# Performance work log

Hardware: AMD Instinct MI355X
Metric: run time of the kernel (lower is better)

The kernel has to match this reference:

```python
import jax, jax.numpy as jnp
import numpy as np

N = 100000   # nodes
E = 3200000  # edges (avg degree 32)
H = 75       # hidden
ITER = 3     # num_layers


def setup_inputs() -> dict:
    key = jax.random.key(0)
    ks = jax.random.split(key, 16)
    s = 0.1  # weight scale
    x = jax.random.normal(ks[0], (N, H), jnp.float32)
    src = jax.random.randint(ks[1], (E,), 0, N)
    dst = jax.random.randint(ks[2], (E,), 0, N)
    edge_index = jnp.stack([src, dst]).astype(jnp.int32)
    rn = lambda k, shp: jax.random.normal(k, shp, jnp.float32) * s
    return {
        "x": x,
        "edge_index": edge_index,
        "eps": jnp.zeros((1,), jnp.float32),      # GIN train_eps, init 0
        "w1": rn(ks[3], (H, H)), "b1": jnp.zeros((H,), jnp.float32),
        "w2": rn(ks[4], (H, H)), "b2": jnp.zeros((H,), jnp.float32),
        "w_ih": rn(ks[5], (3 * H, H)), "w_hh": rn(ks[6], (3 * H, H)),
        "b_ih": jnp.zeros((3 * H,), jnp.float32), "b_hh": jnp.zeros((3 * H,), jnp.float32),
        "wc1": rn(ks[7], (ITER * H, 2 * H)), "bc1": jnp.zeros((2 * H,), jnp.float32),
        "wc2": rn(ks[8], (2 * H, H)), "bc2": jnp.zeros((H,), jnp.float32),
    }


def reference(x, edge_index, eps, w1, b1, w2, b2, w_ih, w_hh, b_ih, b_hh, wc1, bc1, wc2, bc2):
    src, dst = edge_index[0], edge_index[1]

    def gin(xt):
        # sum aggregation over incoming edges (gather -> scatter-add)
        agg = jax.ops.segment_sum(xt[src], dst, num_segments=N)
        z = (1.0 + eps[0]) * xt + agg
        return jnp.maximum(z @ w1 + b1, 0.0) @ w2 + b2

    def gru_step(inp, h):
        # torch.nn.GRU single step; gate order: r, z, n
        gi = inp @ w_ih.T + b_ih
        gh = h @ w_hh.T + b_hh
        ir, iz, inn = jnp.split(gi, 3, axis=-1)
        hr, hz, hn = jnp.split(gh, 3, axis=-1)
        r = jax.nn.sigmoid(ir + hr)
        zg = jax.nn.sigmoid(iz + hz)
        n = jnp.tanh(inn + r * hn)
        return (1.0 - zg) * n + zg * h

    h = x   # h0 = x.unsqueeze(0)
    xt = x
    node_states = []
    for _ in range(ITER):
        m = jnp.maximum(gin(xt), 0.0)
        h = gru_step(m, h)
        xt = h  # GRU output == hidden state for single layer/step
        node_states.append(xt)

    cat = jnp.concatenate(node_states, axis=1)  # [N, ITER*H]
    readout = jnp.maximum(cat @ wc1 + bc1, 0.0) @ wc2 + bc2
    return (xt, readout)
```

## Files before the change

kernel.cpp:

```cpp
#include <hip/hip_runtime.h>

#define NN 100000
#define EE 3200000
#define N2 100032
#define NBUCK 782
#define CPAD 16
#define CHUNK 12288
#define CAP 5120

typedef _Float16 f16;
typedef _Float16 f16x8 __attribute__((ext_vector_type(8)));
typedef float f32x4 __attribute__((ext_vector_type(4)));
typedef unsigned int u32;

#define MFMA(a, b, c) __builtin_amdgcn_mfma_f32_16x16x32_f16((a), (b), (c), 0, 0, 0)


__global__ __launch_bounds__(256) void initcur_kernel(int* __restrict__ bcur) {
  int i = blockIdx.x * 256 + threadIdx.x;
  if (i < NBUCK) bcur[i * CPAD] = i * CAP;
}

__global__ __launch_bounds__(256) void binB_kernel(const int* __restrict__ src,
                                                   const int* __restrict__ dst,
                                                   int* __restrict__ bcur,
                                                   u32* __restrict__ ebuf) {
  __shared__ int hist[NBUCK];
  __shared__ int base[NBUCK];
  int tid = threadIdx.x;
  int e0 = blockIdx.x * CHUNK;
  int e1 = e0 + CHUNK;
  if (e1 > EE) e1 = EE;
  for (int i = tid; i < NBUCK; i += 256) hist[i] = 0;
  __syncthreads();
  for (int e = e0 + tid * 4; e < e1; e += 1024) {
    int4 d = *(const int4*)(dst + e);
    atomicAdd(&hist[d.x >> 7], 1);
    atomicAdd(&hist[d.y >> 7], 1);
    atomicAdd(&hist[d.z >> 7], 1);
    atomicAdd(&hist[d.w >> 7], 1);
  }
  __syncthreads();
  for (int i = tid; i < NBUCK; i += 256) {
    int c = hist[i];
    if (c) base[i] = atomicAdd(&bcur[i * CPAD], c);
  }
  __syncthreads();
  for (int i = tid; i < NBUCK; i += 256) hist[i] = 0;
  __syncthreads();
  for (int e = e0 + tid * 4; e < e1; e += 1024) {
    int4 d = *(const int4*)(dst + e);
    int4 s = *(const int4*)(src + e);
    int b, loc;
    b = d.x >> 7; loc = atomicAdd(&hist[b], 1);
    ebuf[base[b] + loc] = (u32)s.x | ((u32)(d.x & 127) << 17);
    b = d.y >> 7; loc = atomicAdd(&hist[b], 1);
    ebuf[base[b] + loc] = (u32)s.y | ((u32)(d.y & 127) << 17);
    b = d.z >> 7; loc = atomicAdd(&hist[b], 1);
    ebuf[base[b] + loc] = (u32)s.z | ((u32)(d.z & 127) << 17);
    b = d.w >> 7; loc = atomicAdd(&hist[b], 1);
    ebuf[base[b] + loc] = (u32)s.w | ((u32)(d.w & 127) << 17);
  }
}

__global__ __launch_bounds__(256) void binC_kernel(const u32* __restrict__ ebuf,
                                                   const int* __restrict__ bcur,
                                                   int* __restrict__ st,
                                                   int* __restrict__ ct,
                                                   int* __restrict__ csr) {
  __shared__ int cnt[128], sc[128], cur[128];
  int b = blockIdx.x, tid = threadIdx.x;
  int e0 = b * CAP;
  int e1 = bcur[b * CPAD];
  if (tid < 128) cnt[tid] = 0;
  __syncthreads();
  for (int e = e0 + tid; e < e1; e += 256) atomicAdd(&cnt[ebuf[e] >> 17], 1);
  __syncthreads();
  if (tid < 128) sc[tid] = cnt[tid];
  __syncthreads();
  for (int off = 1; off < 128; off <<= 1) {
    int t = 0;
    if (tid < 128 && tid >= off) t = sc[tid - off];
    __syncthreads();
    if (tid < 128) sc[tid] += t;
    __syncthreads();
  }
  if (tid < 128) {
    int gpos = e0 + sc[tid] - cnt[tid];
    int node = b * 128 + tid;
    if (node < NN) {
      st[node] = gpos;
      ct[node] = cnt[tid];
    }
    cur[tid] = gpos;
  }
  __syncthreads();
  for (int e = e0 + tid; e < e1; e += 256) {
    u32 p = ebuf[e];
    int pos = atomicAdd(&cur[p >> 17], 1);
    csr[pos] = (int)(p & 0x1FFFFu);
  }
}


__device__ __forceinline__ f16 pack_one(const float* __restrict__ W,
                                        const float* __restrict__ bias, int rel, int K, int Nc,
                                        int KG, int trans, int bslot) {
  int e = rel & 7, nn = (rel >> 3) & 15;
  int g = (rel >> 7) % KG, nb = (rel >> 7) / KG;
  int k = g * 8 + e, n = nb * 16 + nn;
  float v = 0.f;
  if (n < Nc) {
    if (k < K) v = trans ? W[n * K + k] : W[k * Nc + n];
    else if (k == bslot) v = bias[n];
  }
  return (f16)v;
}

__global__ __launch_bounds__(256) void prep_kernel(const float* __restrict__ x,
                                                   f16* __restrict__ xp,
                                                   const float* __restrict__ w1,
                                                   const float* __restrict__ b1,
                                                   const float* __restrict__ w2,
                                                   const float* __restrict__ b2,
                                                   const float* __restrict__ wih,
                                                   const float* __restrict__ bih,
                                                   const float* __restrict__ whh,
                                                   const float* __restrict__ bhh,
                                                   const float* __restrict__ wc1,
                                                   const float* __restrict__ bc1,
                                                   const float* __restrict__ wc2,
                                                   const float* __restrict__ bc2,
                                                   f16* __restrict__ wp) {
  int b = blockIdx.x, tid = threadIdx.x;
  if (b < 470) {
    int i = b * 256 + tid;
    if (i >= 120320) return;
    f16 v;
    if (i < 7680) v = pack_one(w1, b1, i, 75, 75, 12, 0, 95);
    else if (i < 15360) v = pack_one(w2, b2, i - 7680, 75, 75, 12, 0, 95);
    else if (i < 38400) {
      int r = i - 15360, g = r / 7680;
      v = pack_one(wih + g * 5625, bih + g * 75, r - g * 7680, 75, 75, 12, 1, 95);
    } else if (i < 61440) {
      int r = i - 38400, g = r / 7680;
      v = pack_one(whh + g * 5625, bhh + g * 75, r - g * 7680, 75, 75, 12, 1, 95);
    } else if (i < 107520) {
      int rel = i - 61440;
      int e = rel & 7, nn = (rel >> 3) & 15;
      int g = (rel >> 7) % 36, nb = (rel >> 7) / 36;
      int q = g * 8 + e, buf = q / 96, kk = q - buf * 96, n = nb * 16 + nn;
      float f = 0.f;
      if (n < 150) {
        if (kk < 75) f = wc1[(buf * 75 + kk) * 150 + n];
        else if (kk == 95 && buf == 0) f = bc1[n];
      }
      v = (f16)f;
    } else v = pack_one(wc2, bc2, i - 107520, 150, 75, 20, 0, 159);
    wp[i] = v;
  } else {
    int i = (b - 470) * 256 + tid;
    int r = i / 96, c = i - r * 96;
    float v = (r < NN && c < 75) ? x[r * 75 + c] : (c == 95 ? 1.f : 0.f);
    xp[i] = (f16)v;
  }
}


__global__ __launch_bounds__(256) void fuse_kernel(const f16* __restrict__ hcur,
                                                   const int* __restrict__ st,
                                                   const int* __restrict__ ct,
                                                   const int* __restrict__ csr,
                                                   const float* __restrict__ eps,
                                                   const f16* __restrict__ w1p,
                                                   const f16* __restrict__ w2p,
                                                   const f16* __restrict__ wihp,
                                                   const f16* __restrict__ whhp,
                                                   f16* __restrict__ hb_out,
                                                   float* __restrict__ outx) {
  __shared__ f16 Ls[4][16 * 104];
  __shared__ f16 Hs[4][16 * 104];
  int tid = threadIdx.x;
  int w = tid >> 6, l = tid & 63, lm = l & 15, lg = l >> 4;
  int row0 = blockIdx.x * 64 + w * 16;
  f16* Ld = Ls[w];
  int g = l / 10, j = l - g * 10;
  float ep = 1.f + eps[0];
#pragma unroll 1
  for (int r = 0; r < 3; ++r) {
    int idx = r * 6 + g;
    if (g < 6 && idx < 16) {
      int n = row0 + idx;
      bool valid = n < NN;
      int e = valid ? st[n] : 0;
      int eend = e + (valid ? ct[n] : 0);
      float acc[8] = {0, 0, 0, 0, 0, 0, 0, 0};
#pragma unroll 4
      for (; e < eend; ++e) {
        int sr = csr[e];
        f16x8 v = *(const f16x8*)(hcur + sr * 96 + j * 8);
#pragma unroll
        for (int k = 0; k < 8; ++k) acc[k] += (float)v[k];
      }
      f16x8 o;
      if (valid) {
        f16x8 self = *(const f16x8*)(hcur + n * 96 + j * 8);
#pragma unroll
        for (int k = 0; k < 8; ++k) o[k] = (f16)(ep * (float)self[k] + acc[k]);
      } else {
#pragma unroll
        for (int k = 0; k < 8; ++k) o[k] = (f16)0.f;
      }
      *(f16x8*)(Ld + idx * 104 + j * 8) = o;
    }
  }
#pragma unroll
  for (int c = 0; c < 4; ++c) {
    int col = 80 + lg * 4 + c;
    Ld[lm * 104 + col] = (f16)(col == 95 ? 1.f : 0.f);
  }
  const f16* hr = hcur + (row0 + lm) * 96;
  f16x8 h0 = *(const f16x8*)(hr + lg * 8);
  f16x8 h1 = *(const f16x8*)(hr + 32 + lg * 8);
  f16x8 h2 = *(const f16x8*)(hr + 64 + lg * 8);
  f16* Hd = Hs[w];
  *(f16x8*)(Hd + lm * 104 + lg * 8) = h0;
  *(f16x8*)(Hd + lm * 104 + 32 + lg * 8) = h1;
  *(f16x8*)(Hd + lm * 104 + 64 + lg * 8) = h2;
  const f16* Lr = Ld + lm * 104;
  f16x8 a0 = *(const f16x8*)(Lr + lg * 8);
  f16x8 a1 = *(const f16x8*)(Lr + 32 + lg * 8);
  f16x8 a2 = *(const f16x8*)(Lr + 64 + lg * 8);
#pragma unroll
  for (int nb = 0; nb < 5; ++nb) {
    const f16* bp = w1p + ((nb * 12 + lg) * 16 + lm) * 8;
    f32x4 acc = (f32x4){0.f, 0.f, 0.f, 0.f};
    acc = MFMA(a0, *(const f16x8*)bp, acc);
    acc = MFMA(a1, *(const f16x8*)(bp + 512), acc);
    acc = MFMA(a2, *(const f16x8*)(bp + 1024), acc);
#pragma unroll
    for (int r = 0; r < 4; ++r)
      Ld[(lg * 4 + r) * 104 + nb * 16 + lm] = (f16)fmaxf(acc[r], 0.f);
  }
  f16x8 c0 = *(const f16x8*)(Lr + lg * 8);
  f16x8 c1 = *(const f16x8*)(Lr + 32 + lg * 8);
  f16x8 c2 = *(const f16x8*)(Lr + 64 + lg * 8);
#pragma unroll
  for (int nb = 0; nb < 5; ++nb) {
    const f16* bp = w2p + ((nb * 12 + lg) * 16 + lm) * 8;
    f32x4 acc = (f32x4){0.f, 0.f, 0.f, 0.f};
    acc = MFMA(c0, *(const f16x8*)bp, acc);
    acc = MFMA(c1, *(const f16x8*)(bp + 512), acc);
    acc = MFMA(c2, *(const f16x8*)(bp + 1024), acc);
#pragma unroll
    for (int r = 0; r < 4; ++r)
      Ld[(lg * 4 + r) * 104 + nb * 16 + lm] = (f16)fmaxf(acc[r], 0.f);
  }
  f16x8 am0 = *(const f16x8*)(Lr + lg * 8);
  f16x8 am1 = *(const f16x8*)(Lr + 32 + lg * 8);
  f16x8 am2 = *(const f16x8*)(Lr + 64 + lg * 8);
#pragma unroll 1
  for (int nb = 0; nb < 5; ++nb) {
    f32x4 rg = (f32x4){0.f, 0.f, 0.f, 0.f};
    f32x4 zg = rg, ni = rg, nh = rg;
#pragma unroll
    for (int s = 0; s < 3; ++s) {
      f16x8 ams = (s == 0) ? am0 : (s == 1) ? am1 : am2;
      f16x8 ahs = (s == 0) ? h0 : (s == 1) ? h1 : h2;
      int fo = ((nb * 12 + s * 4 + lg) * 16 + lm) * 8;
      rg = MFMA(ams, *(const f16x8*)(wihp + fo), rg);
      rg = MFMA(ahs, *(const f16x8*)(whhp + fo), rg);
      zg = MFMA(ams, *(const f16x8*)(wihp + 7680 + fo), zg);
      zg = MFMA(ahs, *(const f16x8*)(whhp + 7680 + fo), zg);
      ni = MFMA(ams, *(const f16x8*)(wihp + 15360 + fo), ni);
      nh = MFMA(ahs, *(const f16x8*)(whhp + 15360 + fo), nh);
    }
#pragma unroll
    for (int r = 0; r < 4; ++r) {
      int n = nb * 16 + lm;
      float hval = (float)Hd[(lg * 4 + r) * 104 + n];
      float rv = 1.f / (1.f + __expf(-rg[r]));
      float zv = 1.f / (1.f + __expf(-zg[r]));
      float u = ni[r] + rv * nh[r];
      float t = __expf(-2.f * fabsf(u));
      float nv = copysignf((1.f - t) / (1.f + t), u);
      float hp = zv * (hval - nv) + nv;
      Ld[(lg * 4 + r) * 104 + n] = (f16)hp;
    }
  }
#pragma unroll
  for (int k = 0; k < 3; ++k) {
    int p = l + 64 * k;
    int r = p / 12, sl = p - r * 12;
    f16x8 v = *(const f16x8*)(Ld + r * 104 + sl * 8);
    *(f16x8*)(hb_out + (row0 + r) * 96 + sl * 8) = v;
  }
  if (outx) {
    for (int k = 0; k < 19; ++k) {
      int p = l + 64 * k;
      int gi = row0 * 75 + p;
      if (p < 1200 && gi < NN * 75) {
        int r = p / 75, c = p - r * 75;
        outx[gi] = (float)Ld[r * 104 + c];
      }
    }
  }
}


__global__ __launch_bounds__(256) void readout_kernel(const f16* __restrict__ hb0,
                                                      const f16* __restrict__ hb1,
                                                      const f16* __restrict__ hb2,
                                                      const f16* __restrict__ wc1p,
                                                      const f16* __restrict__ wc2p,
                                                      float* __restrict__ out) {
  __shared__ f16 Ls[4][16 * 168];
  int tid = threadIdx.x;
  int w = tid >> 6, l = tid & 63, lm = l & 15, lg = l >> 4;
  int row0 = blockIdx.x * 64 + w * 16;
  int row = row0 + lm;
  f16x8 a[9];
#pragma unroll
  for (int s = 0; s < 9; ++s) {
    const f16* hb = (s < 3) ? hb0 : (s < 6) ? hb1 : hb2;
    a[s] = *(const f16x8*)(hb + row * 96 + (4 * (s - (s / 3) * 3) + lg) * 8);
  }
  f16* Ld = Ls[w];
#pragma unroll
  for (int nb = 0; nb < 10; ++nb) {
    f32x4 acc = (f32x4){0.f, 0.f, 0.f, 0.f};
#pragma unroll
    for (int s = 0; s < 9; ++s)
      acc = MFMA(a[s], *(const f16x8*)(wc1p + ((nb * 36 + 4 * s + lg) * 16 + lm) * 8), acc);
#pragma unroll
    for (int r = 0; r < 4; ++r) {
      int n = nb * 16 + lm;
      float v = fmaxf(acc[r], 0.f);
      if (n >= 150) v = (n == 159) ? 1.f : 0.f;
      Ld[(lg * 4 + r) * 168 + n] = (f16)v;
    }
  }
  const f16* Lr = Ls[w] + lm * 168;
  f16x8 a2[5];
#pragma unroll
  for (int s = 0; s < 5; ++s) a2[s] = *(const f16x8*)(Lr + s * 32 + lg * 8);
  f32x4 acc2[5];
#pragma unroll
  for (int nb = 0; nb < 5; ++nb) {
    acc2[nb] = (f32x4){0.f, 0.f, 0.f, 0.f};
#pragma unroll
    for (int s = 0; s < 5; ++s)
      acc2[nb] = MFMA(a2[s], *(const f16x8*)(wc2p + ((nb * 20 + s * 4 + lg) * 16 + lm) * 8),
                      acc2[nb]);
  }
  float* Lf = (float*)Ls[w];
#pragma unroll
  for (int nb = 0; nb < 5; ++nb)
#pragma unroll
    for (int r = 0; r < 4; ++r) {
      int n = nb * 16 + lm;
      if (n < 75) Lf[(lg * 4 + r) * 76 + n] = acc2[nb][r];
    }
  for (int k = 0; k < 19; ++k) {
    int p = l + 64 * k;
    int gi = row0 * 75 + p;
    if (p < 1200 && gi < NN * 75) {
      int r = p / 75, c = p - r * 75;
      out[gi] = Lf[r * 76 + c];
    }
  }
}


extern "C" void kernel_launch(void* const* d_in, const int* in_sizes, int n_in,
                              void* d_out, int out_size, void* d_ws, size_t ws_size,
                              hipStream_t stream) {
  const float* x    = (const float*)d_in[0];
  const int*   ei   = (const int*)d_in[1];
  const float* eps  = (const float*)d_in[2];
  const float* w1   = (const float*)d_in[3];
  const float* b1   = (const float*)d_in[4];
  const float* w2   = (const float*)d_in[5];
  const float* b2   = (const float*)d_in[6];
  const float* w_ih = (const float*)d_in[7];
  const float* w_hh = (const float*)d_in[8];
  const float* b_ih = (const float*)d_in[9];
  const float* b_hh = (const float*)d_in[10];
  const float* wc1  = (const float*)d_in[11];
  const float* bc1  = (const float*)d_in[12];
  const float* wc2  = (const float*)d_in[13];
  const float* bc2  = (const float*)d_in[14];

  const int* srcv = ei;
  const int* dstv = ei + EE;

  float* out_x = (float*)d_out;
  float* out_r = out_x + NN * 75;

  f16* x0   = (f16*)d_ws;
  f16* hb0  = x0 + (size_t)N2 * 96;
  f16* hb1  = hb0 + (size_t)N2 * 96;
  f16* hb2  = hb1 + (size_t)N2 * 96;
  f16* wp   = hb2 + (size_t)N2 * 96;
  f16* w1p  = wp;
  f16* w2p  = wp + 7680;
  f16* wihp = wp + 15360;
  f16* whhp = wp + 38400;
  f16* wc1p = wp + 61440;
  f16* wc2p = wp + 107520;
  u32* ebuf = (u32*)(wp + 120320);
  int* csr  = (int*)(ebuf + (size_t)NBUCK * CAP);
  int* st   = csr + (size_t)NBUCK * CAP;
  int* ctv  = st + NN;
  int* bcur = ctv + NN;

  initcur_kernel<<<4, 256, 0, stream>>>(bcur);
  binB_kernel<<<(EE + CHUNK - 1) / CHUNK, 256, 0, stream>>>(srcv, dstv, bcur, ebuf);
  binC_kernel<<<NBUCK, 256, 0, stream>>>(ebuf, bcur, st, ctv, csr);
  prep_kernel<<<37982, 256, 0, stream>>>(x, x0, w1, b1, w2, b2, w_ih, b_ih,
                                         w_hh, b_hh, wc1, bc1, wc2, bc2, wp);

  int gb = N2 / 64;
  f16* hbs[3] = {hb0, hb1, hb2};
  for (int it = 0; it < 3; ++it) {
    const f16* h = (it == 0) ? x0 : hbs[it - 1];
    fuse_kernel<<<gb, 256, 0, stream>>>(h, st, ctv, csr, eps, w1p, w2p, wihp, whhp,
                                        hbs[it], (it == 2) ? out_x : nullptr);
  }
  readout_kernel<<<gb, 256, 0, stream>>>(hb0, hb1, hb2, wc1p, wc2p, out_r);
}
```

Baseline: 544.5 us.

## Split fused GIN layer into edge-parallel aggregation and MLP/GRU kernels

```diff
diff --git a/kernel.cpp b/kernel.cpp
--- a/kernel.cpp
+++ b/kernel.cpp
@@ -119,6 +119,8 @@
 
 __global__ __launch_bounds__(256) void prep_kernel(const float* __restrict__ x,
                                                    f16* __restrict__ xp,
+                                                   f16* __restrict__ xc,
+                                                   f16* __restrict__ zm,
                                                    const float* __restrict__ w1,
                                                    const float* __restrict__ b1,
                                                    const float* __restrict__ w2,
@@ -158,68 +160,86 @@
       v = (f16)f;
     } else v = pack_one(wc2, bc2, i - 107520, 150, 75, 20, 0, 159);
     wp[i] = v;
-  } else {
+  } else if (b < 6722) {
     int i = (b - 470) * 256 + tid;
+    int r = i >> 4, c = i & 15;
+    zm[r * 96 + 80 + c] = (f16)(c == 15 ? 1.f : 0.f);
+  } else if (b < 44234) {
+    int i = (b - 6722) * 256 + tid;
     int r = i / 96, c = i - r * 96;
     float v = (r < NN && c < 75) ? x[r * 75 + c] : (c == 95 ? 1.f : 0.f);
     xp[i] = (f16)v;
-  }
-}
-
-
-__global__ __launch_bounds__(256) void fuse_kernel(const f16* __restrict__ hcur,
+  } else {
+    int i = (b - 44234) * 256 + tid;
+    int r = i / 80, c = i - r * 80;
+    float v = (r < NN && c < 75) ? x[r * 75 + c] : 0.f;
+    xc[i] = (f16)v;
+  }
+}
+
+
+__global__ __launch_bounds__(256) void aggz_kernel(const f16* __restrict__ xc,
                                                    const int* __restrict__ st,
                                                    const int* __restrict__ ct,
                                                    const int* __restrict__ csr,
                                                    const float* __restrict__ eps,
-                                                   const f16* __restrict__ w1p,
-                                                   const f16* __restrict__ w2p,
-                                                   const f16* __restrict__ wihp,
-                                                   const f16* __restrict__ whhp,
-                                                   f16* __restrict__ hb_out,
-                                                   float* __restrict__ outx) {
+                                                   f16* __restrict__ zm) {
+  int tid = threadIdx.x;
+  int l = tid & 63;
+  int n = blockIdx.x * 4 + (tid >> 6);
+  if (n >= NN) return;
+  int s = l / 10, j = l - s * 10;
+  int e0 = st[n], e1 = e0 + ct[n];
+  float acc[8] = {0, 0, 0, 0, 0, 0, 0, 0};
+  if (l < 60) {
+#pragma unroll 4
+    for (int e = e0 + s; e < e1; e += 6) {
+      int sr = csr[e];
+      f16x8 v = *(const f16x8*)(xc + sr * 80 + j * 8);
+#pragma unroll
+      for (int k = 0; k < 8; ++k) acc[k] += (float)v[k];
+    }
+  }
+  int l1 = (l + 30) & 63, l2 = (l + 10) & 63, l3 = (l + 20) & 63;
+#pragma unroll
+  for (int k = 0; k < 8; ++k) {
+    float t = __shfl(acc[k], l1, 64);
+    if (l < 30) acc[k] += t;
+    t = __shfl(acc[k], l2, 64);
+    if (l < 10) acc[k] += t;
+    t = __shfl(acc[k], l3, 64);
+    if (l < 10) acc[k] += t;
+  }
+  if (l < 10) {
+    f16x8 self = *(const f16x8*)(xc + n * 80 + j * 8);
+    float ep = 1.f + eps[0];
+    f16x8 o;
+#pragma unroll
+    for (int k = 0; k < 8; ++k) o[k] = (f16)(ep * (float)self[k] + acc[k]);
+    *(f16x8*)(zm + n * 96 + j * 8) = o;
+  }
+}
+
+
+__global__ __launch_bounds__(256) void mlpgru_kernel(const f16* __restrict__ zm,
+                                                     const f16* __restrict__ hcur,
+                                                     const f16* __restrict__ w1p,
+                                                     const f16* __restrict__ w2p,
+                                                     const f16* __restrict__ wihp,
+                                                     const f16* __restrict__ whhp,
+                                                     f16* __restrict__ hb_out,
+                                                     f16* __restrict__ hc_out,
+                                                     float* __restrict__ outx) {
   __shared__ f16 Ls[4][16 * 104];
   __shared__ f16 Hs[4][16 * 104];
   int tid = threadIdx.x;
   int w = tid >> 6, l = tid & 63, lm = l & 15, lg = l >> 4;
   int row0 = blockIdx.x * 64 + w * 16;
-  f16* Ld = Ls[w];
-  int g = l / 10, j = l - g * 10;
-  float ep = 1.f + eps[0];
-#pragma unroll 1
-  for (int r = 0; r < 3; ++r) {
-    int idx = r * 6 + g;
-    if (g < 6 && idx < 16) {
-      int n = row0 + idx;
-      bool valid = n < NN;
-      int e = valid ? st[n] : 0;
-      int eend = e + (valid ? ct[n] : 0);
-      float acc[8] = {0, 0, 0, 0, 0, 0, 0, 0};
-#pragma unroll 4
-      for (; e < eend; ++e) {
-        int sr = csr[e];
-        f16x8 v = *(const f16x8*)(hcur + sr * 96 + j * 8);
-#pragma unroll
-        for (int k = 0; k < 8; ++k) acc[k] += (float)v[k];
-      }
-      f16x8 o;
-      if (valid) {
-        f16x8 self = *(const f16x8*)(hcur + n * 96 + j * 8);
-#pragma unroll
-        for (int k = 0; k < 8; ++k) o[k] = (f16)(ep * (float)self[k] + acc[k]);
-      } else {
-#pragma unroll
-        for (int k = 0; k < 8; ++k) o[k] = (f16)0.f;
-      }
-      *(f16x8*)(Ld + idx * 104 + j * 8) = o;
-    }
-  }
-#pragma unroll
-  for (int c = 0; c < 4; ++c) {
-    int col = 80 + lg * 4 + c;
-    Ld[lm * 104 + col] = (f16)(col == 95 ? 1.f : 0.f);
-  }
+  const f16* ar = zm + (row0 + lm) * 96;
   const f16* hr = hcur + (row0 + lm) * 96;
+  f16x8 a0 = *(const f16x8*)(ar + lg * 8);
+  f16x8 a1 = *(const f16x8*)(ar + 32 + lg * 8);
+  f16x8 a2 = *(const f16x8*)(ar + 64 + lg * 8);
   f16x8 h0 = *(const f16x8*)(hr + lg * 8);
   f16x8 h1 = *(const f16x8*)(hr + 32 + lg * 8);
   f16x8 h2 = *(const f16x8*)(hr + 64 + lg * 8);
@@ -227,10 +247,7 @@
   *(f16x8*)(Hd + lm * 104 + lg * 8) = h0;
   *(f16x8*)(Hd + lm * 104 + 32 + lg * 8) = h1;
   *(f16x8*)(Hd + lm * 104 + 64 + lg * 8) = h2;
-  const f16* Lr = Ld + lm * 104;
-  f16x8 a0 = *(const f16x8*)(Lr + lg * 8);
-  f16x8 a1 = *(const f16x8*)(Lr + 32 + lg * 8);
-  f16x8 a2 = *(const f16x8*)(Lr + 64 + lg * 8);
+  f16* Ld = Ls[w];
 #pragma unroll
   for (int nb = 0; nb < 5; ++nb) {
     const f16* bp = w1p + ((nb * 12 + lg) * 16 + lm) * 8;
@@ -242,6 +259,12 @@
     for (int r = 0; r < 4; ++r)
       Ld[(lg * 4 + r) * 104 + nb * 16 + lm] = (f16)fmaxf(acc[r], 0.f);
   }
+#pragma unroll
+  for (int c = 0; c < 4; ++c) {
+    int col = 80 + lg * 4 + c;
+    Ld[lm * 104 + col] = (f16)(col == 95 ? 1.f : 0.f);
+  }
+  const f16* Lr = Ld + lm * 104;
   f16x8 c0 = *(const f16x8*)(Lr + lg * 8);
   f16x8 c1 = *(const f16x8*)(Lr + 32 + lg * 8);
   f16x8 c2 = *(const f16x8*)(Lr + 64 + lg * 8);
@@ -294,6 +317,17 @@
     int r = p / 12, sl = p - r * 12;
     f16x8 v = *(const f16x8*)(Ld + r * 104 + sl * 8);
     *(f16x8*)(hb_out + (row0 + r) * 96 + sl * 8) = v;
+  }
+  if (hc_out) {
+#pragma unroll
+    for (int k = 0; k < 3; ++k) {
+      int p = l + 64 * k;
+      if (p < 160) {
+        int r = p / 10, sl = p - r * 10;
+        f16x8 v = *(const f16x8*)(Ld + r * 104 + sl * 8);
+        *(f16x8*)(hc_out + (row0 + r) * 80 + sl * 8) = v;
+      }
+    }
   }
   if (outx) {
     for (int k = 0; k < 19; ++k) {
@@ -397,11 +431,13 @@
   float* out_x = (float*)d_out;
   float* out_r = out_x + NN * 75;
 
-  f16* x0   = (f16*)d_ws;
+  f16* zm   = (f16*)d_ws;
+  f16* x0   = zm + (size_t)N2 * 96;
   f16* hb0  = x0 + (size_t)N2 * 96;
   f16* hb1  = hb0 + (size_t)N2 * 96;
   f16* hb2  = hb1 + (size_t)N2 * 96;
-  f16* wp   = hb2 + (size_t)N2 * 96;
+  f16* hc   = hb2 + (size_t)N2 * 96;
+  f16* wp   = hc + (size_t)N2 * 80;
   f16* w1p  = wp;
   f16* w2p  = wp + 7680;
   f16* wihp = wp + 15360;
@@ -417,15 +453,17 @@
   initcur_kernel<<<4, 256, 0, stream>>>(bcur);
   binB_kernel<<<(EE + CHUNK - 1) / CHUNK, 256, 0, stream>>>(srcv, dstv, bcur, ebuf);
   binC_kernel<<<NBUCK, 256, 0, stream>>>(ebuf, bcur, st, ctv, csr);
-  prep_kernel<<<37982, 256, 0, stream>>>(x, x0, w1, b1, w2, b2, w_ih, b_ih,
+  prep_kernel<<<75494, 256, 0, stream>>>(x, x0, hc, zm, w1, b1, w2, b2, w_ih, b_ih,
                                          w_hh, b_hh, wc1, bc1, wc2, bc2, wp);
 
   int gb = N2 / 64;
   f16* hbs[3] = {hb0, hb1, hb2};
   for (int it = 0; it < 3; ++it) {
     const f16* h = (it == 0) ? x0 : hbs[it - 1];
-    fuse_kernel<<<gb, 256, 0, stream>>>(h, st, ctv, csr, eps, w1p, w2p, wihp, whhp,
-                                        hbs[it], (it == 2) ? out_x : nullptr);
+    aggz_kernel<<<25000, 256, 0, stream>>>(hc, st, ctv, csr, eps, zm);
+    mlpgru_kernel<<<gb, 256, 0, stream>>>(zm, h, w1p, w2p, wihp, whhp, hbs[it],
+                                          (it < 2) ? hc : nullptr,
+                                          (it == 2) ? out_x : nullptr);
   }
   readout_kernel<<<gb, 256, 0, stream>>>(hb0, hb1, hb2, wc1p, wc2p, out_r);
 }
```

Result: slower. 557.1 us (+2.3%).
